# Optimization experiments

Measured on AMD Instinct MI355X. Metric: run time of the kernel, lower is better.

Reference implementation:

```python
import jax, jax.numpy as jnp
import numpy as np

B, H, SQ, SK, D = 2, 16, 2048, 2048, 128
P_DROP = 0.5


def setup_inputs() -> dict:
    key = jax.random.key(0)
    kq, kk, kv, km = jax.random.split(key, 4)
    query = jax.random.normal(kq, (B, H, SQ, D), dtype=jnp.float32)
    key_t = jax.random.normal(kk, (B, H, SK, D), dtype=jnp.float32)
    value = jax.random.normal(kv, (B, H, SK, D), dtype=jnp.float32)
    # deterministic Bernoulli(0.5) keep-mask standing in for dropout(p=0.5, train=True)
    dropout_mask = jax.random.randint(km, (B, H, SQ, SK), 0, 2, dtype=jnp.int32)
    return {"query": query, "key": key_t, "value": value, "dropout_mask": dropout_mask}


def reference(query, key, value, dropout_mask):
    d = query.shape[-1]
    # original: scaled_qk = qk.div(d ** -0.5)  ==  qk * sqrt(d)  (faithful to source)
    scale = jnp.asarray(d, query.dtype) ** 0.5
    qk = jnp.einsum("bhqd,bhkd->bhqk", query, key)  # [B,H,SQ,SK]
    scaled_qk = qk * scale
    keep_scale = jnp.asarray(1.0 / (1.0 - P_DROP), query.dtype)
    dropped = jnp.where(dropout_mask == 1, scaled_qk * keep_scale, jnp.zeros((), query.dtype))
    out = jnp.einsum("bhqk,bhkd->bhqd", dropped, value)  # [B,H,SQ,D]
    return out
```

## Files before the change

### kernel.cpp

```cpp
#include <hip/hip_runtime.h>
#include <hip/hip_bf16.h>

#define B_   2
#define H_   16
#define SQ_  2048
#define SK_  2048
#define D_   128

#define QT   128
#define KT   64
#define NITER (SK_/KT)

using bf16x8 = __attribute__((ext_vector_type(8))) __bf16;
using bf16x4 = __attribute__((ext_vector_type(4))) __bf16;
using f32x4  = __attribute__((ext_vector_type(4))) float;

#define MFMA16(a,b,c) __builtin_amdgcn_mfma_f32_16x16x32_bf16(a,b,c,0,0,0)

#define QK_PITCH 136
#define VT_PITCH 72
#define P_PITCH  72
#define M8_PITCH 72

#define KLDS_BYTES (KT  * QK_PITCH * 2)
#define VT_BYTES   (D_  * VT_PITCH * 2)
#define P_BYTES    (QT  * P_PITCH  * 2)
#define M8_BYTES   (QT  * M8_PITCH)
#define SMEM_BYTES (KLDS_BYTES + VT_BYTES + P_BYTES + M8_BYTES)

__global__ __launch_bounds__(512, 4)
void attn_drop_kernel(const float* __restrict__ Q,
                      const float* __restrict__ K,
                      const float* __restrict__ V,
                      const int*   __restrict__ M,
                      float* __restrict__ Out)
{
    __shared__ __align__(16) char smem[SMEM_BYTES];
    __bf16*  Qs  = (__bf16*)smem;
    __bf16*  Ks  = (__bf16*)smem;
    __bf16*  Vt  = (__bf16*)(smem + KLDS_BYTES);
    __bf16*  Ps  = (__bf16*)(smem + KLDS_BYTES + VT_BYTES);
    unsigned char* Ms8 = (unsigned char*)(smem + KLDS_BYTES + VT_BYTES + P_BYTES);

    const int tid  = threadIdx.x;
    const int wave = tid >> 6;
    const int lane = tid & 63;
    const int quad = lane >> 4;
    const int ln   = lane & 15;

    const int orig = ((blockIdx.x & 7) << 6) | (blockIdx.x >> 3);
    const int bh = orig >> 4;
    const int qb = orig & 15;

    const float* qptr = Q + ((size_t)bh*SQ_ + (size_t)qb*QT) * D_;
    const float* kptr = K + (size_t)bh*SK_*D_;
    const float* vptr = V + (size_t)bh*SK_*D_;
    const int*   mptr = M + (size_t)bh*(size_t)SQ_*SK_ + (size_t)qb*QT*SK_;
    float*       optr = Out + ((size_t)bh*SQ_ + (size_t)qb*QT) * D_;

    const int c  = tid & 31;
    const int g  = tid >> 5;
    const int mc = tid & 15;
    const int mg = tid >> 4;

    float4 kpre[4], vpre[4];
    int4   mpre[4];

    auto load_tile = [&](int kt) {
        const float4* ks = (const float4*)(kptr + (size_t)kt*KT*D_);
        const float4* vs = (const float4*)(vptr + (size_t)kt*KT*D_);
        #pragma unroll
        for (int p = 0; p < 4; ++p) kpre[p] = ks[(g + 16*p)*32 + c];
        #pragma unroll
        for (int i = 0; i < 4; ++i) vpre[i] = vs[(4*g + i)*32 + c];
        const int* mrow = mptr + kt*KT + 4*mc;
        #pragma unroll
        for (int p = 0; p < 4; ++p)
            mpre[p] = *(const int4*)(mrow + (size_t)(mg + 32*p)*SK_);
    };

    auto write_tile = [&]() {
        #pragma unroll
        for (int p = 0; p < 4; ++p) {
            float4 v = kpre[p];
            bf16x4 h = { (__bf16)v.x, (__bf16)v.y, (__bf16)v.z, (__bf16)v.w };
            *(bf16x4*)&Ks[(g + 16*p)*QK_PITCH + 4*c] = h;
        }
        const float* ff = (const float*)vpre;
        #pragma unroll
        for (int j = 0; j < 4; ++j) {
            bf16x4 row = { (__bf16)ff[0*4+j], (__bf16)ff[1*4+j],
                           (__bf16)ff[2*4+j], (__bf16)ff[3*4+j] };
            *(bf16x4*)&Vt[(4*c + j)*VT_PITCH + 4*g] = row;
        }
        #pragma unroll
        for (int p = 0; p < 4; ++p) {
            int4 m = mpre[p];
            unsigned pk = (unsigned)(m.x & 1) | ((unsigned)(m.y & 1) << 8)
                        | ((unsigned)(m.z & 1) << 16) | ((unsigned)(m.w & 1) << 24);
            *(unsigned*)&Ms8[(mg + 32*p)*M8_PITCH + 4*mc] = pk;
        }
    };

    load_tile(0);

    {
        const float4* src = (const float4*)qptr;
        #pragma unroll
        for (int p = 0; p < 8; ++p) {
            int r = g + 16*p;
            float4 v = src[r*32 + c];
            bf16x4 h = { (__bf16)v.x, (__bf16)v.y, (__bf16)v.z, (__bf16)v.w };
            *(bf16x4*)&Qs[r*QK_PITCH + 4*c] = h;
        }
    }
    __syncthreads();

    bf16x8 qf[4];
    #pragma unroll
    for (int s = 0; s < 4; ++s)
        qf[s] = *(const bf16x8*)&Qs[(16*wave + ln)*QK_PITCH + 32*s + 8*quad];

    f32x4 Oacc[8];
    #pragma unroll
    for (int dt = 0; dt < 8; ++dt)
        Oacc[dt] = (f32x4){0.f, 0.f, 0.f, 0.f};

    for (int kt = 0; kt < NITER; ++kt) {
        __syncthreads();
        write_tile();
        __syncthreads();
        if (kt + 1 < NITER) load_tile(kt + 1);

        f32x4 S[4];
        #pragma unroll
        for (int ct = 0; ct < 4; ++ct)
            S[ct] = (f32x4){0.f, 0.f, 0.f, 0.f};

        __builtin_amdgcn_s_setprio(1);
        #pragma unroll
        for (int s = 0; s < 4; ++s) {
            #pragma unroll
            for (int ct = 0; ct < 4; ++ct) {
                bf16x8 kf = *(const bf16x8*)&Ks[(16*ct + ln)*QK_PITCH + 32*s + 8*quad];
                S[ct] = MFMA16(qf[s], kf, S[ct]);
            }
        }
        __builtin_amdgcn_s_setprio(0);

        #pragma unroll
        for (int ct = 0; ct < 4; ++ct) {
            int row0 = 16*wave + 4*quad;
            int col  = 16*ct + ln;
            #pragma unroll
            for (int r = 0; r < 4; ++r) {
                float pv = Ms8[(row0 + r)*M8_PITCH + col] ? S[ct][r] : 0.0f;
                Ps[(row0 + r)*P_PITCH + col] = (__bf16)pv;
            }
        }

        __builtin_amdgcn_s_setprio(1);
        #pragma unroll
        for (int ks = 0; ks < 2; ++ks) {
            bf16x8 pf = *(const bf16x8*)&Ps[(16*wave + ln)*P_PITCH + 32*ks + 8*quad];
            #pragma unroll
            for (int dt = 0; dt < 8; ++dt) {
                bf16x8 vf = *(const bf16x8*)&Vt[(16*dt + ln)*VT_PITCH + 32*ks + 8*quad];
                Oacc[dt] = MFMA16(pf, vf, Oacc[dt]);
            }
        }
        __builtin_amdgcn_s_setprio(0);
    }

    const float SCALE = 22.62741699796952f;
    #pragma unroll
    for (int dt = 0; dt < 8; ++dt) {
        int row0 = 16*wave + 4*quad;
        #pragma unroll
        for (int r = 0; r < 4; ++r)
            optr[(size_t)(row0 + r)*D_ + 16*dt + ln] = Oacc[dt][r] * SCALE;
    }
}

extern "C" void kernel_launch(void* const* d_in, const int* in_sizes, int n_in,
                              void* d_out, int out_size, void* d_ws, size_t ws_size,
                              hipStream_t stream) {
    (void)in_sizes; (void)n_in; (void)d_ws; (void)ws_size; (void)out_size;
    const float* Q = (const float*)d_in[0];
    const float* K = (const float*)d_in[1];
    const float* V = (const float*)d_in[2];
    const int*   M = (const int*)d_in[3];
    float* Out = (float*)d_out;

    dim3 grid(B_ * H_ * (SQ_ / QT));
    attn_drop_kernel<<<grid, 512, 0, stream>>>(Q, K, V, M, Out);
}
```

Baseline: 948.0 us.

## Double-buffer K/V/mask LDS tiles with smaller key tile and swizzled V

Halves the key tile to 32 and double-buffers the K, transposed V and mask tiles in LDS, which removes one __syncthreads per iteration. Q fragments are now loaded straight from global into registers instead of staging through LDS. The transposed V writes and reads use an XOR swizzle to cut LDS bank conflicts. In exchange there are twice as many iterations, each with less MFMA work to hide the global loads. The P buffer is still single-buffered, with only one barrier per iteration guarding it.

```diff
diff --git a/kernel.cpp b/kernel.cpp
--- a/kernel.cpp
+++ b/kernel.cpp
@@ -8,25 +8,26 @@
 #define D_   128
 
 #define QT   128
-#define KT   64
+#define KT   32
 #define NITER (SK_/KT)
 
 using bf16x8 = __attribute__((ext_vector_type(8))) __bf16;
 using bf16x4 = __attribute__((ext_vector_type(4))) __bf16;
+using bf16x2 = __attribute__((ext_vector_type(2))) __bf16;
 using f32x4  = __attribute__((ext_vector_type(4))) float;
 
 #define MFMA16(a,b,c) __builtin_amdgcn_mfma_f32_16x16x32_bf16(a,b,c,0,0,0)
 
-#define QK_PITCH 136
-#define VT_PITCH 72
-#define P_PITCH  72
-#define M8_PITCH 72
+#define K_PITCH  136
+#define VT_PITCH 40
+#define P_PITCH  40
+#define M8_PITCH 40
 
-#define KLDS_BYTES (KT  * QK_PITCH * 2)
-#define VT_BYTES   (D_  * VT_PITCH * 2)
-#define P_BYTES    (QT  * P_PITCH  * 2)
-#define M8_BYTES   (QT  * M8_PITCH)
-#define SMEM_BYTES (KLDS_BYTES + VT_BYTES + P_BYTES + M8_BYTES)
+#define KB_   (KT*K_PITCH*2)
+#define VTB_  (D_*VT_PITCH*2)
+#define M8B_  (QT*M8_PITCH)
+#define PSB_  (QT*P_PITCH*2)
+#define SMEM_BYTES (2*KB_ + 2*VTB_ + 2*M8B_ + PSB_)
 
 __global__ __launch_bounds__(512, 4)
 void attn_drop_kernel(const float* __restrict__ Q,
@@ -36,11 +37,7 @@
                       float* __restrict__ Out)
 {
     __shared__ __align__(16) char smem[SMEM_BYTES];
-    __bf16*  Qs  = (__bf16*)smem;
-    __bf16*  Ks  = (__bf16*)smem;
-    __bf16*  Vt  = (__bf16*)(smem + KLDS_BYTES);
-    __bf16*  Ps  = (__bf16*)(smem + KLDS_BYTES + VT_BYTES);
-    unsigned char* Ms8 = (unsigned char*)(smem + KLDS_BYTES + VT_BYTES + P_BYTES);
+    __bf16* Ps = (__bf16*)(smem + 2*KB_ + 2*VTB_ + 2*M8B_);
 
     const int tid  = threadIdx.x;
     const int wave = tid >> 6;
@@ -60,114 +57,113 @@
 
     const int c  = tid & 31;
     const int g  = tid >> 5;
-    const int mc = tid & 15;
-    const int mg = tid >> 4;
+    const int mc = tid & 7;
+    const int mg = tid >> 3;
 
-    float4 kpre[4], vpre[4];
-    int4   mpre[4];
+    const int wxor = (2*g) ^ ((c & 3) * 8);
+    const int vrd  = 8 * (quad ^ ((ln >> 2) & 3));
+
+    float4 kpre0, kpre1, vpre0, vpre1;
+    int4   mpre0, mpre1;
 
     auto load_tile = [&](int kt) {
         const float4* ks = (const float4*)(kptr + (size_t)kt*KT*D_);
         const float4* vs = (const float4*)(vptr + (size_t)kt*KT*D_);
-        #pragma unroll
-        for (int p = 0; p < 4; ++p) kpre[p] = ks[(g + 16*p)*32 + c];
-        #pragma unroll
-        for (int i = 0; i < 4; ++i) vpre[i] = vs[(4*g + i)*32 + c];
+        kpre0 = ks[g*32 + c];
+        kpre1 = ks[(g+16)*32 + c];
+        vpre0 = vs[(2*g  )*32 + c];
+        vpre1 = vs[(2*g+1)*32 + c];
         const int* mrow = mptr + kt*KT + 4*mc;
-        #pragma unroll
-        for (int p = 0; p < 4; ++p)
-            mpre[p] = *(const int4*)(mrow + (size_t)(mg + 32*p)*SK_);
+        mpre0 = *(const int4*)(mrow + (size_t)mg*SK_);
+        mpre1 = *(const int4*)(mrow + (size_t)(mg+64)*SK_);
     };
 
-    auto write_tile = [&]() {
-        #pragma unroll
-        for (int p = 0; p < 4; ++p) {
-            float4 v = kpre[p];
-            bf16x4 h = { (__bf16)v.x, (__bf16)v.y, (__bf16)v.z, (__bf16)v.w };
-            *(bf16x4*)&Ks[(g + 16*p)*QK_PITCH + 4*c] = h;
+    auto write_tile = [&](int b) {
+        __bf16* ksb = (__bf16*)(smem + b*KB_);
+        __bf16* vtb = (__bf16*)(smem + 2*KB_ + b*VTB_);
+        unsigned char* msb = (unsigned char*)(smem + 2*KB_ + 2*VTB_ + b*M8B_);
+        {
+            bf16x4 h0 = { (__bf16)kpre0.x, (__bf16)kpre0.y, (__bf16)kpre0.z, (__bf16)kpre0.w };
+            bf16x4 h1 = { (__bf16)kpre1.x, (__bf16)kpre1.y, (__bf16)kpre1.z, (__bf16)kpre1.w };
+            *(bf16x4*)&ksb[ g      *K_PITCH + 4*c] = h0;
+            *(bf16x4*)&ksb[(g+16)  *K_PITCH + 4*c] = h1;
         }
-        const float* ff = (const float*)vpre;
-        #pragma unroll
-        for (int j = 0; j < 4; ++j) {
-            bf16x4 row = { (__bf16)ff[0*4+j], (__bf16)ff[1*4+j],
-                           (__bf16)ff[2*4+j], (__bf16)ff[3*4+j] };
-            *(bf16x4*)&Vt[(4*c + j)*VT_PITCH + 4*g] = row;
+        {
+            const float* f0 = (const float*)&vpre0;
+            const float* f1 = (const float*)&vpre1;
+            #pragma unroll
+            for (int j = 0; j < 4; ++j) {
+                bf16x2 pr = { (__bf16)f0[j], (__bf16)f1[j] };
+                *(bf16x2*)&vtb[(4*c + j)*VT_PITCH + wxor] = pr;
+            }
         }
-        #pragma unroll
-        for (int p = 0; p < 4; ++p) {
-            int4 m = mpre[p];
-            unsigned pk = (unsigned)(m.x & 1) | ((unsigned)(m.y & 1) << 8)
-                        | ((unsigned)(m.z & 1) << 16) | ((unsigned)(m.w & 1) << 24);
-            *(unsigned*)&Ms8[(mg + 32*p)*M8_PITCH + 4*mc] = pk;
+        {
+            unsigned pk0 = (unsigned)(mpre0.x & 1) | ((unsigned)(mpre0.y & 1) << 8)
+                         | ((unsigned)(mpre0.z & 1) << 16) | ((unsigned)(mpre0.w & 1) << 24);
+            unsigned pk1 = (unsigned)(mpre1.x & 1) | ((unsigned)(mpre1.y & 1) << 8)
+                         | ((unsigned)(mpre1.z & 1) << 16) | ((unsigned)(mpre1.w & 1) << 24);
+            *(unsigned*)&msb[ mg      *M8_PITCH + 4*mc] = pk0;
+            *(unsigned*)&msb[(mg+64)  *M8_PITCH + 4*mc] = pk1;
         }
     };
 
     load_tile(0);
 
+    bf16x8 qf[4];
     {
-        const float4* src = (const float4*)qptr;
+        const float* qrow = qptr + (size_t)(16*wave + ln)*D_;
         #pragma unroll
-        for (int p = 0; p < 8; ++p) {
-            int r = g + 16*p;
-            float4 v = src[r*32 + c];
-            bf16x4 h = { (__bf16)v.x, (__bf16)v.y, (__bf16)v.z, (__bf16)v.w };
-            *(bf16x4*)&Qs[r*QK_PITCH + 4*c] = h;
+        for (int s = 0; s < 4; ++s) {
+            float4 a = *(const float4*)(qrow + 32*s + 8*quad);
+            float4 b2 = *(const float4*)(qrow + 32*s + 8*quad + 4);
+            qf[s] = (bf16x8){ (__bf16)a.x, (__bf16)a.y, (__bf16)a.z, (__bf16)a.w,
+                              (__bf16)b2.x, (__bf16)b2.y, (__bf16)b2.z, (__bf16)b2.w };
         }
     }
-    __syncthreads();
-
-    bf16x8 qf[4];
-    #pragma unroll
-    for (int s = 0; s < 4; ++s)
-        qf[s] = *(const bf16x8*)&Qs[(16*wave + ln)*QK_PITCH + 32*s + 8*quad];
 
     f32x4 Oacc[8];
     #pragma unroll
     for (int dt = 0; dt < 8; ++dt)
         Oacc[dt] = (f32x4){0.f, 0.f, 0.f, 0.f};
 
+    const int row0 = 16*wave + 4*quad;
+
     for (int kt = 0; kt < NITER; ++kt) {
-        __syncthreads();
-        write_tile();
+        const int b = kt & 1;
+        write_tile(b);
         __syncthreads();
         if (kt + 1 < NITER) load_tile(kt + 1);
 
-        f32x4 S[4];
-        #pragma unroll
-        for (int ct = 0; ct < 4; ++ct)
-            S[ct] = (f32x4){0.f, 0.f, 0.f, 0.f};
+        const __bf16* ksb = (const __bf16*)(smem + b*KB_);
+        const __bf16* vtb = (const __bf16*)(smem + 2*KB_ + b*VTB_);
+        const unsigned char* msb = (const unsigned char*)(smem + 2*KB_ + 2*VTB_ + b*M8B_);
 
+        f32x4 S0 = (f32x4){0.f,0.f,0.f,0.f};
+        f32x4 S1 = (f32x4){0.f,0.f,0.f,0.f};
         __builtin_amdgcn_s_setprio(1);
         #pragma unroll
         for (int s = 0; s < 4; ++s) {
-            #pragma unroll
-            for (int ct = 0; ct < 4; ++ct) {
-                bf16x8 kf = *(const bf16x8*)&Ks[(16*ct + ln)*QK_PITCH + 32*s + 8*quad];
-                S[ct] = MFMA16(qf[s], kf, S[ct]);
-            }
+            bf16x8 kf0 = *(const bf16x8*)&ksb[ ln      *K_PITCH + 32*s + 8*quad];
+            bf16x8 kf1 = *(const bf16x8*)&ksb[(16+ln)  *K_PITCH + 32*s + 8*quad];
+            S0 = MFMA16(qf[s], kf0, S0);
+            S1 = MFMA16(qf[s], kf1, S1);
         }
         __builtin_amdgcn_s_setprio(0);
 
         #pragma unroll
-        for (int ct = 0; ct < 4; ++ct) {
-            int row0 = 16*wave + 4*quad;
-            int col  = 16*ct + ln;
-            #pragma unroll
-            for (int r = 0; r < 4; ++r) {
-                float pv = Ms8[(row0 + r)*M8_PITCH + col] ? S[ct][r] : 0.0f;
-                Ps[(row0 + r)*P_PITCH + col] = (__bf16)pv;
-            }
+        for (int r = 0; r < 4; ++r) {
+            float p0 = msb[(row0 + r)*M8_PITCH + ln     ] ? S0[r] : 0.0f;
+            float p1 = msb[(row0 + r)*M8_PITCH + 16 + ln] ? S1[r] : 0.0f;
+            Ps[(row0 + r)*P_PITCH + ln     ] = (__bf16)p0;
+            Ps[(row0 + r)*P_PITCH + 16 + ln] = (__bf16)p1;
         }
 
+        bf16x8 pf = *(const bf16x8*)&Ps[(16*wave + ln)*P_PITCH + 8*quad];
         __builtin_amdgcn_s_setprio(1);
         #pragma unroll
-        for (int ks = 0; ks < 2; ++ks) {
-            bf16x8 pf = *(const bf16x8*)&Ps[(16*wave + ln)*P_PITCH + 32*ks + 8*quad];
-            #pragma unroll
-            for (int dt = 0; dt < 8; ++dt) {
-                bf16x8 vf = *(const bf16x8*)&Vt[(16*dt + ln)*VT_PITCH + 32*ks + 8*quad];
-                Oacc[dt] = MFMA16(pf, vf, Oacc[dt]);
-            }
+        for (int dt = 0; dt < 8; ++dt) {
+            bf16x8 vf = *(const bf16x8*)&vtb[(16*dt + ln)*VT_PITCH + vrd];
+            Oacc[dt] = MFMA16(pf, vf, Oacc[dt]);
         }
         __builtin_amdgcn_s_setprio(0);
     }
@@ -175,7 +171,6 @@
     const float SCALE = 22.62741699796952f;
     #pragma unroll
     for (int dt = 0; dt < 8; ++dt) {
-        int row0 = 16*wave + 4*quad;
         #pragma unroll
         for (int r = 0; r < 4; ++r)
             optr[(size_t)(row0 + r)*D_ + 16*dt + ln] = Oacc[dt][r] * SCALE;
```

Measured after the change: 786.7 us. 1.21x faster.
